# Kernel tuning notes

Hardware: AMD Instinct MI355X
Metric: run time of the kernel (lower is better)

## Reference

```python
import jax, jax.numpy as jnp
import numpy as np

D_MODEL = 1024
NUM_HEADS = 16
D_K = D_MODEL // NUM_HEADS
B, T = 2, 2048


def setup_inputs() -> dict:
    key = jax.random.key(0)
    ks = jax.random.split(key, 11)
    s = 1.0 / np.sqrt(D_MODEL)
    inp = {
        "query": jax.random.normal(ks[0], (B, T, D_MODEL), jnp.float32),
        "key_in": jax.random.normal(ks[1], (B, T, D_MODEL), jnp.float32),
        "value": jax.random.normal(ks[2], (B, T, D_MODEL), jnp.float32),
        "Wq": jax.random.uniform(ks[3], (D_MODEL, D_MODEL), jnp.float32, -s, s),
        "bq": jax.random.uniform(ks[4], (D_MODEL,), jnp.float32, -s, s),
        "Wk": jax.random.uniform(ks[5], (D_MODEL, D_MODEL), jnp.float32, -s, s),
        "bk": jax.random.uniform(ks[6], (D_MODEL,), jnp.float32, -s, s),
        "Wv": jax.random.uniform(ks[7], (D_MODEL, D_MODEL), jnp.float32, -s, s),
        "bv": jax.random.uniform(ks[8], (D_MODEL,), jnp.float32, -s, s),
        "Wo": jax.random.uniform(ks[9], (D_MODEL, D_MODEL), jnp.float32, -s, s),
        "bo": jax.random.uniform(ks[10], (D_MODEL,), jnp.float32, -s, s),
    }
    return inp


def reference(query, key_in, value, Wq, bq, Wk, bk, Wv, bv, Wo, bo):
    Bz, Tz, Dz = query.shape
    # QKV projections (torch Linear: x @ W.T + b)
    q = (query @ Wq.T + bq).reshape(Bz, Tz, NUM_HEADS, D_K).transpose(0, 2, 1, 3)
    k = (key_in @ Wk.T + bk).reshape(Bz, Tz, NUM_HEADS, D_K).transpose(0, 2, 1, 3)
    v = (value @ Wv.T + bv).reshape(Bz, Tz, NUM_HEADS, D_K).transpose(0, 2, 1, 3)
    # full O(T^2) score matrix, as in the original module
    scores = jnp.einsum("bhtd,bhsd->bhts", q, k) / jnp.sqrt(jnp.float32(D_K)).astype(q.dtype)
    attn = jax.nn.softmax(scores, axis=-1)
    context = jnp.einsum("bhts,bhsd->bhtd", attn, v)
    context = context.transpose(0, 2, 1, 3).reshape(Bz, Tz, Dz)
    return context @ Wo.T + bo
```

## Files before the change

kernel.cpp:

```cpp
#include <hip/hip_runtime.h>

typedef unsigned short ushort_t;
typedef __attribute__((ext_vector_type(8))) short bf16x8;
typedef __attribute__((ext_vector_type(4))) float f32x4;

#define DMODEL 1024
#define NHEADS 16
#define DK 64
#define BS 2
#define TS 2048
#define MROWS (BS * TS)

#define QSCALE 0.1803368801111204f

__device__ __forceinline__ ushort_t f2bf(float x) {
    unsigned u = __float_as_uint(x);
    return (ushort_t)((u + 0x7FFFu + ((u >> 16) & 1u)) >> 16);
}

__device__ __forceinline__ unsigned cvt_pk_bf16(float lo, float hi) {
    unsigned r;
    asm("v_cvt_pk_bf16_f32 %0, %1, %2" : "=v"(r) : "v"(lo), "v"(hi));
    return r;
}

__device__ __forceinline__ void gload_lds16(const void* g, void* l) {
    __builtin_amdgcn_global_load_lds(
        (const __attribute__((address_space(1))) unsigned*)g,
        (__attribute__((address_space(3))) unsigned*)l, 16, 0, 0);
}

__global__ __launch_bounds__(256) void cvt_all_kernel(
    const float* __restrict__ q, const float* __restrict__ k,
    const float* __restrict__ v, const float* __restrict__ wq,
    const float* __restrict__ wk, const float* __restrict__ wv,
    const float* __restrict__ wo, ushort_t* __restrict__ dst)
{
    const int i = blockIdx.x * 256 + threadIdx.x;
    const float4* s;
    int off;
    if (i < (1 << 20))      { s = (const float4*)q; off = i; }
    else if (i < (2 << 20)) { s = (const float4*)k; off = i - (1 << 20); }
    else if (i < (3 << 20)) { s = (const float4*)v; off = i - (2 << 20); }
    else {
        const int j = i - (3 << 20);
        const int w = j >> 18;
        off = j & 0x3FFFF;
        s = (w == 0) ? (const float4*)wq : (w == 1) ? (const float4*)wk
          : (w == 2) ? (const float4*)wv : (const float4*)wo;
    }
    const float4 x = s[off];
    ushort4 o;
    o.x = f2bf(x.x); o.y = f2bf(x.y); o.z = f2bf(x.z); o.w = f2bf(x.w);
    ((ushort4*)dst)[i] = o;
}

template <bool SWAP>
__device__ __forceinline__ void gemm_body128(
    const ushort_t* __restrict__ A, const ushort_t* __restrict__ W,
    ushort_t (&Asm)[2][4096], ushort_t (&Bsm)[2][4096],
    f32x4 (&acc)[4][4], int row0, int col0, int w, int lane)
{
    const int c = lane & 15, g = lane >> 4;
    const int wr = w >> 1, wc = w & 1;
    const int lr = lane >> 2;
    const int lcb = (lane & 3) * 8;
    const ushort_t* Ab = &A[(size_t)(row0 + w * 32 + lr) * DMODEL + lcb];
    const ushort_t* Wb = &W[(size_t)(col0 + w * 32 + lr) * DMODEL + lcb];

#define GSTAGE(buf, k0_) do { \
    gload_lds16(Ab + (k0_), &Asm[buf][(w * 32) * 32]); \
    gload_lds16(Ab + 16 * DMODEL + (k0_), &Asm[buf][(w * 32 + 16) * 32]); \
    gload_lds16(Wb + (k0_), &Bsm[buf][(w * 32) * 32]); \
    gload_lds16(Wb + 16 * DMODEL + (k0_), &Bsm[buf][(w * 32 + 16) * 32]); \
} while (0)

    GSTAGE(0, 0);
    __syncthreads();
    int cur = 0;
    for (int k0 = 0; k0 < DMODEL; k0 += 32) {
        if (k0 + 32 < DMODEL) GSTAGE(cur ^ 1, k0 + 32);
        bf16x8 a[4], b[4];
#pragma unroll
        for (int m = 0; m < 4; ++m)
            a[m] = *(const bf16x8*)&Asm[cur][(wr * 64 + m * 16 + c) * 32 + g * 8];
#pragma unroll
        for (int n = 0; n < 4; ++n)
            b[n] = *(const bf16x8*)&Bsm[cur][(wc * 64 + n * 16 + c) * 32 + g * 8];
        __builtin_amdgcn_s_setprio(1);
#pragma unroll
        for (int m = 0; m < 4; ++m)
#pragma unroll
            for (int n = 0; n < 4; ++n)
                acc[m][n] = SWAP
                    ? __builtin_amdgcn_mfma_f32_16x16x32_bf16(b[n], a[m],
                                                              acc[m][n], 0, 0, 0)
                    : __builtin_amdgcn_mfma_f32_16x16x32_bf16(a[m], b[n],
                                                              acc[m][n], 0, 0, 0);
        __builtin_amdgcn_s_setprio(0);
        __syncthreads();
        cur ^= 1;
    }
#undef GSTAGE
}

__global__ __launch_bounds__(256) void gemm_qkv_kernel(
    const ushort_t* __restrict__ Aq, const ushort_t* __restrict__ Ak,
    const ushort_t* __restrict__ Av, const ushort_t* __restrict__ Wq,
    const ushort_t* __restrict__ Wk, const ushort_t* __restrict__ Wv,
    const float* __restrict__ bq, const float* __restrict__ bk,
    const float* __restrict__ bv, ushort_t* __restrict__ Qo,
    ushort_t* __restrict__ Ko, ushort_t* __restrict__ VTo)
{
    __shared__ ushort_t Asm[2][4096];
    __shared__ ushort_t Bsm[2][4096];

    const int z = blockIdx.z;
    const ushort_t* A = (z == 0) ? Aq : (z == 1) ? Ak : Av;
    const ushort_t* W = (z == 0) ? Wq : (z == 1) ? Wk : Wv;
    const float* bias = (z == 0) ? bq : (z == 1) ? bk : bv;

    const int tid = threadIdx.x, w = tid >> 6, lane = tid & 63;
    const int c = lane & 15, g = lane >> 4;
    const int wr = w >> 1, wc = w & 1;
    const int row0 = blockIdx.y * 128, col0 = blockIdx.x * 128;

    f32x4 acc[4][4];
#pragma unroll
    for (int m = 0; m < 4; ++m)
#pragma unroll
        for (int n = 0; n < 4; ++n) acc[m][n] = (f32x4){0.f, 0.f, 0.f, 0.f};

    const int gc0 = col0 + wc * 64;

    if (z < 2) {
        gemm_body128<true>(A, W, Asm, Bsm, acc, row0, col0, w, lane);
        const float scale = (z == 0) ? QSCALE : 1.0f;
        ushort_t* O = (z == 0) ? Qo : Ko;
        float4 bias4[4];
#pragma unroll
        for (int n = 0; n < 4; ++n)
            bias4[n] = *(const float4*)&bias[gc0 + n * 16 + g * 4];
#pragma unroll
        for (int m = 0; m < 4; ++m) {
            const int gr = row0 + wr * 64 + m * 16 + c;
            const int bb = gr >> 11, t = gr & 2047;
#pragma unroll
            for (int n = 0; n < 4; ++n) {
                const int col = gc0 + n * 16 + g * 4;
                const int h = col >> 6, dk0 = col & 63;
                uint2 u;
                u.x = cvt_pk_bf16((acc[m][n][0] + bias4[n].x) * scale,
                                  (acc[m][n][1] + bias4[n].y) * scale);
                u.y = cvt_pk_bf16((acc[m][n][2] + bias4[n].z) * scale,
                                  (acc[m][n][3] + bias4[n].w) * scale);
                *(uint2*)&O[(((size_t)(bb * NHEADS + h) * TS + t) << 6) + dk0] = u;
            }
        }
    } else {
        gemm_body128<false>(A, W, Asm, Bsm, acc, row0, col0, w, lane);
        float bv4[4];
#pragma unroll
        for (int n = 0; n < 4; ++n) bv4[n] = bias[gc0 + n * 16 + c];
#pragma unroll
        for (int m = 0; m < 4; ++m) {
            const int gr0 = row0 + wr * 64 + m * 16 + g * 4;
            const int bb = gr0 >> 11, t0 = gr0 & 2047;
#pragma unroll
            for (int n = 0; n < 4; ++n) {
                const int gc = gc0 + n * 16 + c;
                const int h = gc >> 6, dk = gc & 63;
                uint2 u;
                u.x = cvt_pk_bf16(acc[m][n][0] + bv4[n],
                                  acc[m][n][1] + bv4[n]);
                u.y = cvt_pk_bf16(acc[m][n][2] + bv4[n],
                                  acc[m][n][3] + bv4[n]);
                *(uint2*)&VTo[((size_t)(bb * NHEADS + h) * DK + dk) * TS + t0] = u;
            }
        }
    }
}

__global__ __launch_bounds__(256) void gemm_out_kernel(
    const ushort_t* __restrict__ A, const ushort_t* __restrict__ W,
    const float* __restrict__ bias, float* __restrict__ Cout)
{
    __shared__ ushort_t Asm[2][4096];
    __shared__ ushort_t Bsm[2][4096];

    const int tid = threadIdx.x, w = tid >> 6, lane = tid & 63;
    const int c = lane & 15, g = lane >> 4;
    const int wr = w >> 1, wc = w & 1;
    const int row0 = blockIdx.y * 128, col0 = blockIdx.x * 128;

    f32x4 acc[4][4];
#pragma unroll
    for (int m = 0; m < 4; ++m)
#pragma unroll
        for (int n = 0; n < 4; ++n) acc[m][n] = (f32x4){0.f, 0.f, 0.f, 0.f};

    gemm_body128<true>(A, W, Asm, Bsm, acc, row0, col0, w, lane);

    const int gc0 = col0 + wc * 64;
    float4 bias4[4];
#pragma unroll
    for (int n = 0; n < 4; ++n)
        bias4[n] = *(const float4*)&bias[gc0 + n * 16 + g * 4];
#pragma unroll
    for (int m = 0; m < 4; ++m) {
        const int gr = row0 + wr * 64 + m * 16 + c;
#pragma unroll
        for (int n = 0; n < 4; ++n) {
            float4 cv;
            cv.x = acc[m][n][0] + bias4[n].x;
            cv.y = acc[m][n][1] + bias4[n].y;
            cv.z = acc[m][n][2] + bias4[n].z;
            cv.w = acc[m][n][3] + bias4[n].w;
            *(float4*)&Cout[(size_t)gr * DMODEL + gc0 + n * 16 + g * 4] = cv;
        }
    }
}

__global__ __launch_bounds__(256) void attn_bf16_kernel(
    const ushort_t* __restrict__ Q, const ushort_t* __restrict__ K,
    const ushort_t* __restrict__ VT, ushort_t* __restrict__ ctx)
{
    __shared__ ushort_t Ks[2][64 * 64];
    __shared__ ushort_t Vt[2][64 * 64];
    __shared__ ushort_t Ps[4][32 * 64];

    const int tid = threadIdx.x;
    const int w = tid >> 6, lane = tid & 63;
    const int c = lane & 15, g = lane >> 4;
    const int sid = blockIdx.x;
    const int bh = (sid & 7) | ((sid >> 7) << 3);
    const int qb = (sid >> 3) & 15;
    const int q0 = qb << 7;
    const size_t base = (size_t)bh * TS * DK;
    const ushort_t* Qp = Q + base;
    const ushort_t* Kp = K + base;
    const ushort_t* VTp = VT + base;

    const int lrow8 = lane >> 3;
    const int lc16 = lane & 7;
    const int scol = (lc16 ^ lrow8) << 3;
    const ushort_t* Kg = Kp + (size_t)(w * 16 + lrow8) * DK + scol;
    const ushort_t* Vg = VTp + (size_t)(w * 16 + lrow8) * TS + scol;

#define STAGE(buf, s0_) do { \
    gload_lds16(Kg + (size_t)(s0_) * DK, &Ks[buf][(w * 16) * 64]); \
    gload_lds16(Kg + (size_t)((s0_) + 8) * DK, &Ks[buf][(w * 16 + 8) * 64]); \
    gload_lds16(Vg + (s0_), &Vt[buf][(w * 16) * 64]); \
    gload_lds16(Vg + (s0_) + 8 * TS, &Vt[buf][(w * 16 + 8) * 64]); \
} while (0)

    bf16x8 qa[2][2];
#pragma unroll
    for (int qh = 0; qh < 2; ++qh) {
        const ushort_t* qrow = Qp + (size_t)(q0 + w * 32 + qh * 16 + c) * DK;
        qa[qh][0] = *(const bf16x8*)(qrow + g * 8);
        qa[qh][1] = *(const bf16x8*)(qrow + 32 + g * 8);
    }

    float m_i[2] = {-1e30f, -1e30f}, l_i[2] = {0.f, 0.f};
    f32x4 o[2][4];
#pragma unroll
    for (int qh = 0; qh < 2; ++qh)
#pragma unroll
        for (int df = 0; df < 4; ++df) o[qh][df] = (f32x4){0.f, 0.f, 0.f, 0.f};

    const int cs = (c & 7) << 4;
    char* Pw0 = (char*)&Ps[w][0];

    STAGE(0, 0);
    __syncthreads();
    int cur = 0;

    for (int s0 = 0; s0 < TS; s0 += 64) {
        if (s0 + 64 < TS) STAGE(cur ^ 1, s0 + 64);

        const char* Kb = (const char*)&Ks[cur][0];
        const char* Vb = (const char*)&Vt[cur][0];

        f32x4 sf[2][4];
#pragma unroll
        for (int qh = 0; qh < 2; ++qh)
#pragma unroll
            for (int fc = 0; fc < 4; ++fc) sf[qh][fc] = (f32x4){0.f, 0.f, 0.f, 0.f};
#pragma unroll
        for (int fc = 0; fc < 4; ++fc) {
#pragma unroll
            for (int ch = 0; ch < 2; ++ch) {
                const bf16x8 kb = *(const bf16x8*)(Kb + (fc * 16 + c) * 128 +
                                                   ((ch * 64 + g * 16) ^ cs));
                __builtin_amdgcn_s_setprio(1);
                sf[0][fc] = __builtin_amdgcn_mfma_f32_16x16x32_bf16(kb, qa[0][ch],
                                                                    sf[0][fc], 0, 0, 0);
                sf[1][fc] = __builtin_amdgcn_mfma_f32_16x16x32_bf16(kb, qa[1][ch],
                                                                    sf[1][fc], 0, 0, 0);
                __builtin_amdgcn_s_setprio(0);
            }
        }

        float mt[2];
#pragma unroll
        for (int qh = 0; qh < 2; ++qh) {
            float a0 = fmaxf(fmaxf(sf[qh][0][0], sf[qh][0][1]),
                             fmaxf(sf[qh][0][2], sf[qh][0][3]));
            float a1 = fmaxf(fmaxf(sf[qh][1][0], sf[qh][1][1]),
                             fmaxf(sf[qh][1][2], sf[qh][1][3]));
            float a2 = fmaxf(fmaxf(sf[qh][2][0], sf[qh][2][1]),
                             fmaxf(sf[qh][2][2], sf[qh][2][3]));
            float a3 = fmaxf(fmaxf(sf[qh][3][0], sf[qh][3][1]),
                             fmaxf(sf[qh][3][2], sf[qh][3][3]));
            float m = fmaxf(fmaxf(a0, a1), fmaxf(a2, a3));
            m = fmaxf(m, __shfl_xor(m, 16));
            m = fmaxf(m, __shfl_xor(m, 32));
            mt[qh] = m;
        }

        const int defer = (mt[0] <= m_i[0] + 8.f) && (mt[1] <= m_i[1] + 8.f);
        if (!__all(defer)) {
#pragma unroll
            for (int qh = 0; qh < 2; ++qh) {
                const float mn = fmaxf(m_i[qh], mt[qh]);
                const float fs = __builtin_amdgcn_exp2f(m_i[qh] - mn);
                m_i[qh] = mn;
                l_i[qh] *= fs;
#pragma unroll
                for (int df = 0; df < 4; ++df)
#pragma unroll
                    for (int r = 0; r < 4; ++r) o[qh][df][r] *= fs;
            }
        }

#pragma unroll
        for (int qh = 0; qh < 2; ++qh) {
            char* Pw = Pw0 + (qh * 16 + c) * 128;
            float rs = 0.f;
#pragma unroll
            for (int fc = 0; fc < 4; ++fc) {
                float p0 = __builtin_amdgcn_exp2f(sf[qh][fc][0] - m_i[qh]);
                float p1 = __builtin_amdgcn_exp2f(sf[qh][fc][1] - m_i[qh]);
                float p2 = __builtin_amdgcn_exp2f(sf[qh][fc][2] - m_i[qh]);
                float p3 = __builtin_amdgcn_exp2f(sf[qh][fc][3] - m_i[qh]);
                rs += (p0 + p1) + (p2 + p3);
                uint2 u;
                u.x = cvt_pk_bf16(p0, p1);
                u.y = cvt_pk_bf16(p2, p3);
                *(uint2*)(Pw + ((fc * 32 + g * 8) ^ cs)) = u;
            }
            rs += __shfl_xor(rs, 16);
            rs += __shfl_xor(rs, 32);
            l_i[qh] += rs;
        }

#pragma unroll
        for (int ch = 0; ch < 2; ++ch) {
            const bf16x8 pb0 = *(const bf16x8*)(Pw0 + c * 128 +
                                                ((ch * 64 + g * 16) ^ cs));
            const bf16x8 pb1 = *(const bf16x8*)(Pw0 + (16 + c) * 128 +
                                                ((ch * 64 + g * 16) ^ cs));
#pragma unroll
            for (int df = 0; df < 4; ++df) {
                const bf16x8 vb = *(const bf16x8*)(Vb + (df * 16 + c) * 128 +
                                                   ((ch * 64 + g * 16) ^ cs));
                __builtin_amdgcn_s_setprio(1);
                o[0][df] = __builtin_amdgcn_mfma_f32_16x16x32_bf16(vb, pb0,
                                                                   o[0][df], 0, 0, 0);
                o[1][df] = __builtin_amdgcn_mfma_f32_16x16x32_bf16(vb, pb1,
                                                                   o[1][df], 0, 0, 0);
                __builtin_amdgcn_s_setprio(0);
            }
        }
        __syncthreads();
        cur ^= 1;
    }
#undef STAGE

    const int bb = bh >> 4, h = bh & 15;
#pragma unroll
    for (int qh = 0; qh < 2; ++qh) {
        const float inv = 1.0f / l_i[qh];
        const int t = q0 + w * 32 + qh * 16 + c;
        ushort_t* crow = ctx + ((size_t)(bb * TS + t) * DMODEL + h * 64 + g * 4);
#pragma unroll
        for (int df = 0; df < 4; ++df) {
            uint2 u;
            u.x = cvt_pk_bf16(o[qh][df][0] * inv, o[qh][df][1] * inv);
            u.y = cvt_pk_bf16(o[qh][df][2] * inv, o[qh][df][3] * inv);
            *(uint2*)(crow + df * 16) = u;
        }
    }
}

extern "C" void kernel_launch(void* const* d_in, const int* in_sizes, int n_in,
                              void* d_out, int out_size, void* d_ws, size_t ws_size,
                              hipStream_t stream)
{
    const float* query  = (const float*)d_in[0];
    const float* key_in = (const float*)d_in[1];
    const float* value  = (const float*)d_in[2];
    const float* Wq = (const float*)d_in[3];
    const float* bq = (const float*)d_in[4];
    const float* Wk = (const float*)d_in[5];
    const float* bk = (const float*)d_in[6];
    const float* Wv = (const float*)d_in[7];
    const float* bv = (const float*)d_in[8];
    const float* Wo = (const float*)d_in[9];
    const float* bo = (const float*)d_in[10];

    ushort_t* W16 = (ushort_t*)d_ws;
    const size_t M1 = 1u << 20;
    ushort_t* qi  = W16;
    ushort_t* ki  = W16 + 4 * M1;
    ushort_t* vi  = W16 + 8 * M1;
    ushort_t* wqb = W16 + 12 * M1;
    ushort_t* wkb = W16 + 13 * M1;
    ushort_t* wvb = W16 + 14 * M1;
    ushort_t* wob = W16 + 15 * M1;
    ushort_t* Qp  = W16 + 16 * M1;
    ushort_t* Kp  = W16 + 20 * M1;
    ushort_t* VpT = W16 + 24 * M1;
    ushort_t* cb  = W16 + 28 * M1;

    cvt_all_kernel<<<16384, 256, 0, stream>>>(query, key_in, value,
                                              Wq, Wk, Wv, Wo, W16);

    gemm_qkv_kernel<<<dim3(8, 32, 3), 256, 0, stream>>>(
        qi, ki, vi, wqb, wkb, wvb, bq, bk, bv, Qp, Kp, VpT);

    attn_bf16_kernel<<<512, 256, 0, stream>>>(Qp, Kp, VpT, cb);

    gemm_out_kernel<<<dim3(8, 32), 256, 0, stream>>>(cb, wob, bo, (float*)d_out);
}
```

Before: 248.1 us.

## Triple-buffer GEMM LDS staging with vmcnt waits and a single barrier

Expands the projection GEMM shared-memory staging from two to three buffers, so loads for tile k+2 are issued while tile k is computed. Each iteration now waits only on the older outstanding global-to-LDS loads via s_waitcnt vmcnt(4) and uses one barrier instead of two __syncthreads. This hides more global load latency and cuts barrier cost, at the price of 50% more LDS per block, which may reduce occupancy.

```diff
diff --git a/kernel.cpp b/kernel.cpp
--- a/kernel.cpp
+++ b/kernel.cpp
@@ -58,7 +58,7 @@
 template <bool SWAP>
 __device__ __forceinline__ void gemm_body128(
     const ushort_t* __restrict__ A, const ushort_t* __restrict__ W,
-    ushort_t (&Asm)[2][4096], ushort_t (&Bsm)[2][4096],
+    ushort_t (&Asm)[3][4096], ushort_t (&Bsm)[3][4096],
     f32x4 (&acc)[4][4], int row0, int col0, int w, int lane)
 {
     const int c = lane & 15, g = lane >> 4;
@@ -67,26 +67,41 @@
     const int lcb = (lane & 3) * 8;
     const ushort_t* Ab = &A[(size_t)(row0 + w * 32 + lr) * DMODEL + lcb];
     const ushort_t* Wb = &W[(size_t)(col0 + w * 32 + lr) * DMODEL + lcb];
+    ushort_t* A0 = &Asm[0][0];
+    ushort_t* B0 = &Bsm[0][0];
 
 #define GSTAGE(buf, k0_) do { \
-    gload_lds16(Ab + (k0_), &Asm[buf][(w * 32) * 32]); \
-    gload_lds16(Ab + 16 * DMODEL + (k0_), &Asm[buf][(w * 32 + 16) * 32]); \
-    gload_lds16(Wb + (k0_), &Bsm[buf][(w * 32) * 32]); \
-    gload_lds16(Wb + 16 * DMODEL + (k0_), &Bsm[buf][(w * 32 + 16) * 32]); \
+    gload_lds16(Ab + (k0_), A0 + (buf) * 4096 + (w * 32) * 32); \
+    gload_lds16(Ab + 16 * DMODEL + (k0_), A0 + (buf) * 4096 + (w * 32 + 16) * 32); \
+    gload_lds16(Wb + (k0_), B0 + (buf) * 4096 + (w * 32) * 32); \
+    gload_lds16(Wb + 16 * DMODEL + (k0_), B0 + (buf) * 4096 + (w * 32 + 16) * 32); \
 } while (0)
 
     GSTAGE(0, 0);
-    __syncthreads();
+    GSTAGE(1, 32);
     int cur = 0;
     for (int k0 = 0; k0 < DMODEL; k0 += 32) {
-        if (k0 + 32 < DMODEL) GSTAGE(cur ^ 1, k0 + 32);
+        if (k0 + 32 < DMODEL)
+            asm volatile("s_waitcnt vmcnt(4)" ::: "memory");
+        else
+            asm volatile("s_waitcnt vmcnt(0)" ::: "memory");
+        __builtin_amdgcn_s_barrier();
+        asm volatile("" ::: "memory");
+
+        if (k0 + 64 < DMODEL) {
+            int nb = cur + 2; if (nb >= 3) nb -= 3;
+            GSTAGE(nb, k0 + 64);
+        }
+
+        const ushort_t* Ac = A0 + cur * 4096;
+        const ushort_t* Bc = B0 + cur * 4096;
         bf16x8 a[4], b[4];
 #pragma unroll
         for (int m = 0; m < 4; ++m)
-            a[m] = *(const bf16x8*)&Asm[cur][(wr * 64 + m * 16 + c) * 32 + g * 8];
+            a[m] = *(const bf16x8*)&Ac[(wr * 64 + m * 16 + c) * 32 + g * 8];
 #pragma unroll
         for (int n = 0; n < 4; ++n)
-            b[n] = *(const bf16x8*)&Bsm[cur][(wc * 64 + n * 16 + c) * 32 + g * 8];
+            b[n] = *(const bf16x8*)&Bc[(wc * 64 + n * 16 + c) * 32 + g * 8];
         __builtin_amdgcn_s_setprio(1);
 #pragma unroll
         for (int m = 0; m < 4; ++m)
@@ -98,8 +113,7 @@
                     : __builtin_amdgcn_mfma_f32_16x16x32_bf16(a[m], b[n],
                                                               acc[m][n], 0, 0, 0);
         __builtin_amdgcn_s_setprio(0);
-        __syncthreads();
-        cur ^= 1;
+        cur += 1; if (cur >= 3) cur -= 3;
     }
 #undef GSTAGE
 }
@@ -112,8 +126,8 @@
     const float* __restrict__ bv, ushort_t* __restrict__ Qo,
     ushort_t* __restrict__ Ko, ushort_t* __restrict__ VTo)
 {
-    __shared__ ushort_t Asm[2][4096];
-    __shared__ ushort_t Bsm[2][4096];
+    __shared__ ushort_t Asm[3][4096];
+    __shared__ ushort_t Bsm[3][4096];
 
     const int z = blockIdx.z;
     const ushort_t* A = (z == 0) ? Aq : (z == 1) ? Ak : Av;
@@ -185,8 +199,8 @@
     const ushort_t* __restrict__ A, const ushort_t* __restrict__ W,
     const float* __restrict__ bias, float* __restrict__ Cout)
 {
-    __shared__ ushort_t Asm[2][4096];
-    __shared__ ushort_t Bsm[2][4096];
+    __shared__ ushort_t Asm[3][4096];
+    __shared__ ushort_t Bsm[3][4096];
 
     const int tid = threadIdx.x, w = tid >> 6, lane = tid & 63;
     const int c = lane & 15, g = lane >> 4;
```

Measured after the change: 262.2 us. 5.7% more time.
